# Kernel tuning notes

Hardware: AMD Instinct MI355X
Metric: run time of the kernel (lower is better)

Reference implementation:

```python
import jax, jax.numpy as jnp
import numpy as np

B, L, D, H = 2, 2048, 1024, 16
HD = D // H  # head_dim = 64


def setup_inputs() -> dict:
    key = jax.random.key(0)
    k1, k2, k3 = jax.random.split(key, 3)
    x = jax.random.normal(k1, (B, L, D), dtype=jnp.float32)
    # nn.Linear(d_model, 3*d_model): weight [3D, D], bias [3D]
    lim = 1.0 / np.sqrt(D)
    W_qkv = jax.random.uniform(k2, (3 * D, D), dtype=jnp.float32, minval=-lim, maxval=lim)
    b_qkv = jax.random.uniform(k3, (3 * D,), dtype=jnp.float32, minval=-lim, maxval=lim)
    return {"x": x, "W_qkv": W_qkv, "b_qkv": b_qkv}


def reference(x, W_qkv, b_qkv):
    b, l, d = x.shape
    qkv = x @ W_qkv.T + b_qkv                      # [b, l, 3d]
    q, k, v = jnp.split(qkv, 3, axis=-1)           # each [b, l, d]
    # split heads: [b, l, h, hd]
    q = q.reshape(b, l, H, HD)
    k = k.reshape(b, l, H, HD)
    v = v.reshape(b, l, H, HD)
    scale = 1.0 / np.sqrt(HD).astype(np.float32)
    # scores [b, h, l, l]
    scores = jnp.einsum('bqhd,bkhd->bhqk', q, k) * scale
    attn = jax.nn.softmax(scores, axis=-1)
    out = jnp.einsum('bhqk,bkhd->bqhd', attn, v)   # [b, l, h, hd]
    return out.reshape(b, l, d)
```

## Files before the change

kernel.cpp:

```cpp
#include <hip/hip_runtime.h>

#define BATCH 2
#define SEQ 2048
#define DMODEL 1024
#define NH 16
#define HD 64
#define M_TOT (BATCH*SEQ)
#define N_TOT (3*DMODEL)
#define K_TOT (DMODEL)
#define NQK   (2*DMODEL)
#define QSCALE 0.18033688011112042f

typedef __attribute__((ext_vector_type(8)))  _Float16 f16x8;
typedef __attribute__((ext_vector_type(4)))  float    f32x4;
typedef __attribute__((ext_vector_type(16))) float    f32x16;

static __device__ __forceinline__ unsigned short f2h(float f) {
  _Float16 h = (_Float16)f;
  return __builtin_bit_cast(unsigned short, h);
}

static __device__ __forceinline__ f32x16 zero16() {
  f32x16 z;
  #pragma unroll
  for (int i = 0; i < 16; ++i) z[i] = 0.f;
  return z;
}

static __device__ __forceinline__ void async16(const unsigned short* g, unsigned short* l) {
  __builtin_amdgcn_global_load_lds(
      (const __attribute__((address_space(1))) unsigned*)g,
      (__attribute__((address_space(3))) unsigned*)l, 16, 0, 0);
}

__global__ __launch_bounds__(256) void cast_f16(
    const float* __restrict__ src, unsigned short* __restrict__ dst, int n8)
{
  int i = blockIdx.x * 256 + threadIdx.x;
  if (i >= n8) return;
  float4 v0 = ((const float4*)src)[2*i];
  float4 v1 = ((const float4*)src)[2*i + 1];
  uint4 pk;
  pk.x = (unsigned)f2h(v0.x) | ((unsigned)f2h(v0.y) << 16);
  pk.y = (unsigned)f2h(v0.z) | ((unsigned)f2h(v0.w) << 16);
  pk.z = (unsigned)f2h(v1.x) | ((unsigned)f2h(v1.y) << 16);
  pk.w = (unsigned)f2h(v1.z) | ((unsigned)f2h(v1.w) << 16);
  ((uint4*)dst)[i] = pk;
}

__global__ __launch_bounds__(256) void qkv_gemm_mfma(
    const unsigned short* __restrict__ Xh,
    const unsigned short* __restrict__ Wh,
    const float* __restrict__ bias,
    unsigned short* __restrict__ QK,
    unsigned short* __restrict__ VT)
{
  __shared__ unsigned short As[128][64];
  __shared__ unsigned short Bs[128][64];

  const int tid  = threadIdx.x;
  const int wave = tid >> 6;
  const int lane = tid & 63;
  const int l15  = lane & 15;
  const int quad = lane >> 4;

  const bool isV = (blockIdx.x >= (NQK/128));
  const int n0 = (isV ? (blockIdx.x - NQK/128) : blockIdx.x) * 128;
  const int m0 = blockIdx.y * 128;

  const unsigned short* Arows = isV ? (Wh + (size_t)(NQK + n0) * K_TOT)
                                    : (Xh + (size_t)m0 * K_TOT);
  const unsigned short* Brows = isV ? (Xh + (size_t)m0 * K_TOT)
                                    : (Wh + (size_t)n0 * K_TOT);

  const int sr = tid >> 3;
  const int sp = tid & 7;
  const int sg = ((sp - sr) & 7) * 8;

  const int wm = (wave & 1) * 64;
  const int wn = (wave >> 1) * 64;

  f32x4 acc[4][4];
  #pragma unroll
  for (int i = 0; i < 4; ++i)
    #pragma unroll
    for (int j = 0; j < 4; ++j) acc[i][j] = (f32x4){0.f,0.f,0.f,0.f};

  for (int k0 = 0; k0 < K_TOT; k0 += 64) {
    __syncthreads();
    #pragma unroll
    for (int s = 0; s < 4; ++s) {
      async16(Arows + (size_t)(s*32 + sr) * K_TOT + k0 + sg, &As[0][0] + s*2048 + tid*8);
      async16(Brows + (size_t)(s*32 + sr) * K_TOT + k0 + sg, &Bs[0][0] + s*2048 + tid*8);
    }
    __syncthreads();

    #pragma unroll
    for (int h = 0; h < 2; ++h) {
      f16x8 af[4], bf[4];
      #pragma unroll
      for (int i = 0; i < 4; ++i) {
        const int r = wm + i*16 + l15;
        af[i] = *(const f16x8*)&As[r][((h*4 + quad + r) & 7) * 8];
      }
      #pragma unroll
      for (int j = 0; j < 4; ++j) {
        const int r = wn + j*16 + l15;
        bf[j] = *(const f16x8*)&Bs[r][((h*4 + quad + r) & 7) * 8];
      }
      #pragma unroll
      for (int i = 0; i < 4; ++i)
        #pragma unroll
        for (int j = 0; j < 4; ++j)
          acc[i][j] = __builtin_amdgcn_mfma_f32_16x16x32_f16(af[i], bf[j], acc[i][j], 0, 0, 0);
    }
  }

  if (!isV) {
    const float sc = (n0 < DMODEL) ? QSCALE : 1.0f;
    float bv[4];
    #pragma unroll
    for (int j = 0; j < 4; ++j) bv[j] = bias[n0 + wn + j*16 + l15];
    #pragma unroll
    for (int i = 0; i < 4; ++i)
      #pragma unroll
      for (int j = 0; j < 4; ++j)
        #pragma unroll
        for (int r = 0; r < 4; ++r) {
          const size_t row = (size_t)(m0 + wm + i*16 + quad*4 + r);
          QK[row * NQK + n0 + wn + j*16 + l15] = f2h((acc[i][j][r] + bv[j]) * sc);
        }
  } else {
    const int bidx  = m0 >> 11;
    const int sbase = (m0 & 2047) + wn;
    #pragma unroll
    for (int i = 0; i < 4; ++i)
      #pragma unroll
      for (int r = 0; r < 4; ++r) {
        const int nn = n0 + wm + i*16 + quad*4 + r;
        const float bb = bias[NQK + nn];
        unsigned short* drow =
            VT + ((size_t)(bidx*NH + (nn >> 6)) * HD + (nn & 63)) * SEQ + sbase;
        #pragma unroll
        for (int j = 0; j < 4; ++j)
          drow[j*16 + l15] = f2h(acc[i][j][r] + bb);
      }
  }
}

__global__ __launch_bounds__(256) void attn_mfma3(
    const unsigned short* __restrict__ QK,
    const unsigned short* __restrict__ VT,
    float* __restrict__ out)
{
  __shared__ unsigned short Ks[2][64][64];
  __shared__ unsigned short Vs[2][64][64];
  __shared__ unsigned short Ps[4][32][72];
  __shared__ float Dn[4][32];

  const int tid  = threadIdx.x;
  const int wv   = tid >> 6;
  const int lane = tid & 63;
  const int l31  = lane & 31;
  const int h32  = lane >> 5;
  const int qsw  = l31 >> 3;

  const int qt = blockIdx.x;
  const int hh = blockIdx.y;
  const int b  = blockIdx.z;
  const int q0 = qt*128 + wv*32;

  f16x8 qf[4];
  {
    const unsigned short* qrow = QK + (size_t)(b*SEQ + q0 + l31) * NQK + hh*HD;
    #pragma unroll
    for (int f = 0; f < 4; ++f)
      qf[f] = *(const f16x8*)(qrow + f*16 + h32*8);
  }

  const unsigned short* Kg = QK + (size_t)b*SEQ*NQK + DMODEL + hh*HD;
  const unsigned short* Vg = VT + (size_t)(b*NH + hh) * HD * SEQ;

  const int sr = tid >> 3;
  const int sp = tid & 7;
  const int sg = ((sp - sr) & 7) * 8;

  const unsigned short* kg0 = Kg + (size_t)sr      * NQK + sg;
  const unsigned short* kg1 = Kg + (size_t)(sr+32) * NQK + sg;
  const unsigned short* vg0 = Vg + (size_t)sr      * SEQ + sg;
  const unsigned short* vg1 = Vg + (size_t)(sr+32) * SEQ + sg;
  unsigned short* kl = &Ks[0][0][0] + tid*8;
  unsigned short* vl = &Vs[0][0][0] + tid*8;

  f32x16 oacc[2];
  oacc[0] = zero16();
  oacc[1] = zero16();
  float dsum = 0.f;

  auto STAGE = [&](int kt, int bb) {
    const size_t krow = (size_t)kt * 64 * NQK;
    const int    kcol = kt * 64;
    async16(kg0 + krow, kl + bb*4096);
    async16(kg1 + krow, kl + bb*4096 + 2048);
    async16(vg0 + kcol, vl + bb*4096);
    async16(vg1 + kcol, vl + bb*4096 + 2048);
  };

  auto COMPUTE = [&](int bb) {
    const unsigned short* ks = &Ks[bb][0][0];
    const unsigned short* vs = &Vs[bb][0][0];

    f32x16 sa[2];
    sa[0] = zero16();
    sa[1] = zero16();
    __builtin_amdgcn_s_setprio(1);
    #pragma unroll
    for (int f = 0; f < 4; ++f) {
      const int g = f*2 + h32;
      #pragma unroll
      for (int kb = 0; kb < 2; ++kb) {
        const int row = kb*32 + l31;
        f16x8 kf = *(const f16x8*)(ks + row*64 + ((g + row) & 7) * 8);
        sa[kb] = __builtin_amdgcn_mfma_f32_32x32x16_f16(kf, qf[f], sa[kb], 0, 0, 0);
      }
    }
    __builtin_amdgcn_s_setprio(0);

    #pragma unroll
    for (int kb = 0; kb < 2; ++kb) {
      #pragma unroll
      for (int g4 = 0; g4 < 4; ++g4) {
        unsigned short hsv[4];
        #pragma unroll
        for (int r = 0; r < 4; ++r) {
          float p = exp2f(sa[kb][g4*4 + r]);
          dsum += p;
          hsv[r] = f2h(p);
        }
        unsigned short* dst =
            &Ps[wv][l31][(((kb*4 + g4) ^ qsw) & 7) * 8 + h32*4];
        uint2 pk;
        pk.x = (unsigned)hsv[0] | ((unsigned)hsv[1] << 16);
        pk.y = (unsigned)hsv[2] | ((unsigned)hsv[3] << 16);
        *(uint2*)dst = pk;
      }
    }

    __builtin_amdgcn_s_setprio(1);
    #pragma unroll
    for (int f = 0; f < 4; ++f) {
      const int g = f*2 + h32;
      f16x8 pf = *(const f16x8*)&Ps[wv][l31][((g ^ qsw) & 7) * 8];
      #pragma unroll
      for (int jd = 0; jd < 2; ++jd) {
        const int row = jd*32 + l31;
        f16x8 vf = *(const f16x8*)(vs + row*64 + ((g + row) & 7) * 8);
        oacc[jd] = __builtin_amdgcn_mfma_f32_32x32x16_f16(pf, vf, oacc[jd], 0, 0, 0);
      }
    }
    __builtin_amdgcn_s_setprio(0);
  };

  STAGE(0, 0);
  for (int kt = 0; kt < SEQ/64 - 1; ++kt) {
    STAGE(kt + 1, (kt + 1) & 1);
    asm volatile("s_waitcnt vmcnt(4)" ::: "memory");
    __builtin_amdgcn_s_barrier();
    COMPUTE(kt & 1);
    asm volatile("" ::: "memory");
    __builtin_amdgcn_s_barrier();
  }
  asm volatile("s_waitcnt vmcnt(0)" ::: "memory");
  __builtin_amdgcn_s_barrier();
  COMPUTE((SEQ/64 - 1) & 1);

  dsum += __shfl_xor(dsum, 32, 64);
  Dn[wv][l31] = 1.f / dsum;

  #pragma unroll
  for (int jd = 0; jd < 2; ++jd) {
    #pragma unroll
    for (int g4 = 0; g4 < 4; ++g4) {
      #pragma unroll
      for (int r = 0; r < 4; ++r) {
        const int qrow = g4*8 + h32*4 + r;
        const float oval = oacc[jd][g4*4 + r] * Dn[wv][qrow];
        out[(size_t)(b*SEQ + q0 + qrow) * DMODEL + hh*HD + jd*32 + l31] = oval;
      }
    }
  }
}

extern "C" void kernel_launch(void* const* d_in, const int* in_sizes, int n_in,
                              void* d_out, int out_size, void* d_ws, size_t ws_size,
                              hipStream_t stream) {
  const float* x    = (const float*)d_in[0];
  const float* W    = (const float*)d_in[1];
  const float* bias = (const float*)d_in[2];
  float* out = (float*)d_out;

  unsigned short* qk = (unsigned short*)d_ws;
  unsigned short* vt = qk + (size_t)M_TOT * NQK;
  unsigned short* xh = vt + (size_t)BATCH * NH * HD * SEQ;
  unsigned short* wh = xh + (size_t)M_TOT * K_TOT;

  cast_f16<<<(M_TOT*K_TOT/8 + 255)/256, 256, 0, stream>>>(x, xh, M_TOT*K_TOT/8);
  cast_f16<<<(N_TOT*K_TOT/8 + 255)/256, 256, 0, stream>>>(W, wh, N_TOT*K_TOT/8);

  dim3 g1(N_TOT/128, M_TOT/128);
  qkv_gemm_mfma<<<g1, 256, 0, stream>>>(xh, wh, bias, qk, vt);

  dim3 g2(SEQ/128, NH, BATCH);
  attn_mfma3<<<g2, 256, 0, stream>>>(qk, vt, out);
}
```

Measured before the change: 186.3 us.

## Double-buffer QKV GEMM K-loop and pass P via lane shuffles instead of LDS

```diff
diff --git a/kernel.cpp b/kernel.cpp
--- a/kernel.cpp
+++ b/kernel.cpp
@@ -18,6 +18,10 @@
 static __device__ __forceinline__ unsigned short f2h(float f) {
   _Float16 h = (_Float16)f;
   return __builtin_bit_cast(unsigned short, h);
+}
+
+static __device__ __forceinline__ unsigned pk2h(float a, float b) {
+  return (unsigned)f2h(a) | ((unsigned)f2h(b) << 16);
 }
 
 static __device__ __forceinline__ f32x16 zero16() {
@@ -55,8 +59,8 @@
     unsigned short* __restrict__ QK,
     unsigned short* __restrict__ VT)
 {
-  __shared__ unsigned short As[128][64];
-  __shared__ unsigned short Bs[128][64];
+  __shared__ unsigned short As[2][128][32];
+  __shared__ unsigned short Bs[2][128][32];
 
   const int tid  = threadIdx.x;
   const int wave = tid >> 6;
@@ -73,9 +77,14 @@
   const unsigned short* Brows = isV ? (Xh + (size_t)m0 * K_TOT)
                                     : (Wh + (size_t)n0 * K_TOT);
 
-  const int sr = tid >> 3;
-  const int sp = tid & 7;
-  const int sg = ((sp - sr) & 7) * 8;
+  const int srow = tid >> 2;
+  const int skc  = (tid & 3) * 8;
+  const unsigned short* Ag0 = Arows + (size_t)srow * K_TOT + skc;
+  const unsigned short* Ag1 = Arows + (size_t)(64 + srow) * K_TOT + skc;
+  const unsigned short* Bg0 = Brows + (size_t)srow * K_TOT + skc;
+  const unsigned short* Bg1 = Brows + (size_t)(64 + srow) * K_TOT + skc;
+  unsigned short* Al = &As[0][0][0] + tid * 8;
+  unsigned short* Bl = &Bs[0][0][0] + tid * 8;
 
   const int wm = (wave & 1) * 64;
   const int wn = (wave >> 1) * 64;
@@ -86,35 +95,41 @@
     #pragma unroll
     for (int j = 0; j < 4; ++j) acc[i][j] = (f32x4){0.f,0.f,0.f,0.f};
 
-  for (int k0 = 0; k0 < K_TOT; k0 += 64) {
-    __syncthreads();
-    #pragma unroll
-    for (int s = 0; s < 4; ++s) {
-      async16(Arows + (size_t)(s*32 + sr) * K_TOT + k0 + sg, &As[0][0] + s*2048 + tid*8);
-      async16(Brows + (size_t)(s*32 + sr) * K_TOT + k0 + sg, &Bs[0][0] + s*2048 + tid*8);
-    }
-    __syncthreads();
-
-    #pragma unroll
-    for (int h = 0; h < 2; ++h) {
-      f16x8 af[4], bf[4];
-      #pragma unroll
-      for (int i = 0; i < 4; ++i) {
-        const int r = wm + i*16 + l15;
-        af[i] = *(const f16x8*)&As[r][((h*4 + quad + r) & 7) * 8];
-      }
-      #pragma unroll
-      for (int j = 0; j < 4; ++j) {
-        const int r = wn + j*16 + l15;
-        bf[j] = *(const f16x8*)&Bs[r][((h*4 + quad + r) & 7) * 8];
-      }
-      #pragma unroll
-      for (int i = 0; i < 4; ++i)
-        #pragma unroll
-        for (int j = 0; j < 4; ++j)
-          acc[i][j] = __builtin_amdgcn_mfma_f32_16x16x32_f16(af[i], bf[j], acc[i][j], 0, 0, 0);
-    }
-  }
+  auto STAGE = [&](int k0, int bb) {
+    async16(Ag0 + k0, Al + bb*4096);
+    async16(Ag1 + k0, Al + bb*4096 + 2048);
+    async16(Bg0 + k0, Bl + bb*4096);
+    async16(Bg1 + k0, Bl + bb*4096 + 2048);
+  };
+
+  auto COMPUTE = [&](int bb) {
+    f16x8 af[4], bf[4];
+    #pragma unroll
+    for (int i = 0; i < 4; ++i)
+      af[i] = *(const f16x8*)&As[bb][wm + i*16 + l15][quad*8];
+    #pragma unroll
+    for (int j = 0; j < 4; ++j)
+      bf[j] = *(const f16x8*)&Bs[bb][wn + j*16 + l15][quad*8];
+    __builtin_amdgcn_s_setprio(1);
+    #pragma unroll
+    for (int i = 0; i < 4; ++i)
+      #pragma unroll
+      for (int j = 0; j < 4; ++j)
+        acc[i][j] = __builtin_amdgcn_mfma_f32_16x16x32_f16(af[i], bf[j], acc[i][j], 0, 0, 0);
+    __builtin_amdgcn_s_setprio(0);
+  };
+
+  STAGE(0, 0);
+  for (int t = 0; t < K_TOT/32 - 1; ++t) {
+    STAGE((t+1)*32, (t+1) & 1);
+    asm volatile("s_waitcnt vmcnt(4)" ::: "memory");
+    __builtin_amdgcn_s_barrier();
+    COMPUTE(t & 1);
+    __builtin_amdgcn_s_barrier();
+  }
+  asm volatile("s_waitcnt vmcnt(0)" ::: "memory");
+  __builtin_amdgcn_s_barrier();
+  COMPUTE((K_TOT/32 - 1) & 1);
 
   if (!isV) {
     const float sc = (n0 < DMODEL) ? QSCALE : 1.0f;
@@ -155,7 +170,6 @@
 {
   __shared__ unsigned short Ks[2][64][64];
   __shared__ unsigned short Vs[2][64][64];
-  __shared__ unsigned short Ps[4][32][72];
   __shared__ float Dn[4][32];
 
   const int tid  = threadIdx.x;
@@ -163,7 +177,6 @@
   const int lane = tid & 63;
   const int l31  = lane & 31;
   const int h32  = lane >> 5;
-  const int qsw  = l31 >> 3;
 
   const int qt = blockIdx.x;
   const int hh = blockIdx.y;
@@ -227,30 +240,32 @@
     __builtin_amdgcn_s_setprio(0);
 
     #pragma unroll
-    for (int kb = 0; kb < 2; ++kb) {
-      #pragma unroll
-      for (int g4 = 0; g4 < 4; ++g4) {
-        unsigned short hsv[4];
-        #pragma unroll
-        for (int r = 0; r < 4; ++r) {
-          float p = exp2f(sa[kb][g4*4 + r]);
-          dsum += p;
-          hsv[r] = f2h(p);
-        }
-        unsigned short* dst =
-            &Ps[wv][l31][(((kb*4 + g4) ^ qsw) & 7) * 8 + h32*4];
-        uint2 pk;
-        pk.x = (unsigned)hsv[0] | ((unsigned)hsv[1] << 16);
-        pk.y = (unsigned)hsv[2] | ((unsigned)hsv[3] << 16);
-        *(uint2*)dst = pk;
-      }
-    }
+    for (int kb = 0; kb < 2; ++kb)
+      #pragma unroll
+      for (int i = 0; i < 16; ++i) {
+        float p = exp2f(sa[kb][i]);
+        dsum += p;
+        sa[kb][i] = p;
+      }
 
     __builtin_amdgcn_s_setprio(1);
     #pragma unroll
     for (int f = 0; f < 4; ++f) {
+      const int kb = f >> 1;
+      const int ge = (f & 1) * 2;
+      unsigned A = pk2h(sa[kb][ge*4+0], sa[kb][ge*4+1]);
+      unsigned B = pk2h(sa[kb][ge*4+2], sa[kb][ge*4+3]);
+      unsigned C = pk2h(sa[kb][ge*4+4], sa[kb][ge*4+5]);
+      unsigned D = pk2h(sa[kb][ge*4+6], sa[kb][ge*4+7]);
+      unsigned t0 = (unsigned)__shfl_xor((int)(h32 ? A : C), 32, 64);
+      unsigned t1 = (unsigned)__shfl_xor((int)(h32 ? B : D), 32, 64);
+      uint4 pw;
+      pw.x = h32 ? t0 : A;
+      pw.y = h32 ? t1 : B;
+      pw.z = h32 ? C : t0;
+      pw.w = h32 ? D : t1;
+      f16x8 pf = __builtin_bit_cast(f16x8, pw);
       const int g = f*2 + h32;
-      f16x8 pf = *(const f16x8*)&Ps[wv][l31][((g ^ qsw) & 7) * 8];
       #pragma unroll
       for (int jd = 0; jd < 2; ++jd) {
         const int row = jd*32 + l31;
@@ -267,7 +282,6 @@
     asm volatile("s_waitcnt vmcnt(4)" ::: "memory");
     __builtin_amdgcn_s_barrier();
     COMPUTE(kt & 1);
-    asm volatile("" ::: "memory");
     __builtin_amdgcn_s_barrier();
   }
   asm volatile("s_waitcnt vmcnt(0)" ::: "memory");
```

Result: slower. 192.6 us (+3.4%).

## Triple-buffer GEMM and attention K/V loads, merge the two cast kernels

Applied to the files above, without the earlier changes.

```diff
diff --git a/kernel.cpp b/kernel.cpp
--- a/kernel.cpp
+++ b/kernel.cpp
@@ -33,19 +33,34 @@
       (__attribute__((address_space(3))) unsigned*)l, 16, 0, 0);
 }
 
-__global__ __launch_bounds__(256) void cast_f16(
-    const float* __restrict__ src, unsigned short* __restrict__ dst, int n8)
+static __device__ __forceinline__ void barrier_fenced() {
+  asm volatile("" ::: "memory");
+  __builtin_amdgcn_sched_barrier(0);
+  __builtin_amdgcn_s_barrier();
+  __builtin_amdgcn_sched_barrier(0);
+  asm volatile("" ::: "memory");
+}
+
+__global__ __launch_bounds__(256) void cast_f16_2(
+    const float* __restrict__ xsrc, const float* __restrict__ wsrc,
+    unsigned short* __restrict__ xdst, unsigned short* __restrict__ wdst,
+    int n8x, int n8tot)
 {
   int i = blockIdx.x * 256 + threadIdx.x;
-  if (i >= n8) return;
-  float4 v0 = ((const float4*)src)[2*i];
-  float4 v1 = ((const float4*)src)[2*i + 1];
+  if (i >= n8tot) return;
+  const float* src;
+  unsigned short* dst;
+  int idx;
+  if (i < n8x) { src = xsrc; dst = xdst; idx = i; }
+  else         { src = wsrc; dst = wdst; idx = i - n8x; }
+  float4 v0 = ((const float4*)src)[2*idx];
+  float4 v1 = ((const float4*)src)[2*idx + 1];
   uint4 pk;
   pk.x = (unsigned)f2h(v0.x) | ((unsigned)f2h(v0.y) << 16);
   pk.y = (unsigned)f2h(v0.z) | ((unsigned)f2h(v0.w) << 16);
   pk.z = (unsigned)f2h(v1.x) | ((unsigned)f2h(v1.y) << 16);
   pk.w = (unsigned)f2h(v1.z) | ((unsigned)f2h(v1.w) << 16);
-  ((uint4*)dst)[i] = pk;
+  ((uint4*)dst)[idx] = pk;
 }
 
 __global__ __launch_bounds__(256) void qkv_gemm_mfma(
@@ -55,8 +70,8 @@
     unsigned short* __restrict__ QK,
     unsigned short* __restrict__ VT)
 {
-  __shared__ unsigned short As[128][64];
-  __shared__ unsigned short Bs[128][64];
+  __shared__ unsigned short As[3][128][32];
+  __shared__ unsigned short Bs[3][128][32];
 
   const int tid  = threadIdx.x;
   const int wave = tid >> 6;
@@ -73,9 +88,14 @@
   const unsigned short* Brows = isV ? (Xh + (size_t)m0 * K_TOT)
                                     : (Wh + (size_t)n0 * K_TOT);
 
-  const int sr = tid >> 3;
-  const int sp = tid & 7;
-  const int sg = ((sp - sr) & 7) * 8;
+  const int srow = tid >> 2;
+  const int skc  = (tid & 3) * 8;
+  const unsigned short* Ag0 = Arows + (size_t)srow * K_TOT + skc;
+  const unsigned short* Ag1 = Arows + (size_t)(64 + srow) * K_TOT + skc;
+  const unsigned short* Bg0 = Brows + (size_t)srow * K_TOT + skc;
+  const unsigned short* Bg1 = Brows + (size_t)(64 + srow) * K_TOT + skc;
+  unsigned short* Al = &As[0][0][0] + tid * 8;
+  unsigned short* Bl = &Bs[0][0][0] + tid * 8;
 
   const int wm = (wave & 1) * 64;
   const int wn = (wave >> 1) * 64;
@@ -86,35 +106,46 @@
     #pragma unroll
     for (int j = 0; j < 4; ++j) acc[i][j] = (f32x4){0.f,0.f,0.f,0.f};
 
-  for (int k0 = 0; k0 < K_TOT; k0 += 64) {
-    __syncthreads();
-    #pragma unroll
-    for (int s = 0; s < 4; ++s) {
-      async16(Arows + (size_t)(s*32 + sr) * K_TOT + k0 + sg, &As[0][0] + s*2048 + tid*8);
-      async16(Brows + (size_t)(s*32 + sr) * K_TOT + k0 + sg, &Bs[0][0] + s*2048 + tid*8);
-    }
-    __syncthreads();
-
-    #pragma unroll
-    for (int h = 0; h < 2; ++h) {
-      f16x8 af[4], bf[4];
-      #pragma unroll
-      for (int i = 0; i < 4; ++i) {
-        const int r = wm + i*16 + l15;
-        af[i] = *(const f16x8*)&As[r][((h*4 + quad + r) & 7) * 8];
-      }
-      #pragma unroll
-      for (int j = 0; j < 4; ++j) {
-        const int r = wn + j*16 + l15;
-        bf[j] = *(const f16x8*)&Bs[r][((h*4 + quad + r) & 7) * 8];
-      }
-      #pragma unroll
-      for (int i = 0; i < 4; ++i)
-        #pragma unroll
-        for (int j = 0; j < 4; ++j)
-          acc[i][j] = __builtin_amdgcn_mfma_f32_16x16x32_f16(af[i], bf[j], acc[i][j], 0, 0, 0);
-    }
-  }
+  auto STAGE = [&](int k0, int bb) {
+    async16(Ag0 + k0, Al + bb*4096);
+    async16(Ag1 + k0, Al + bb*4096 + 2048);
+    async16(Bg0 + k0, Bl + bb*4096);
+    async16(Bg1 + k0, Bl + bb*4096 + 2048);
+  };
+
+  auto COMPUTE = [&](int bb) {
+    f16x8 af[4], bf[4];
+    #pragma unroll
+    for (int i = 0; i < 4; ++i)
+      af[i] = *(const f16x8*)&As[bb][wm + i*16 + l15][quad*8];
+    #pragma unroll
+    for (int j = 0; j < 4; ++j)
+      bf[j] = *(const f16x8*)&Bs[bb][wn + j*16 + l15][quad*8];
+    #pragma unroll
+    for (int i = 0; i < 4; ++i)
+      #pragma unroll
+      for (int j = 0; j < 4; ++j)
+        acc[i][j] = __builtin_amdgcn_mfma_f32_16x16x32_f16(af[i], bf[j], acc[i][j], 0, 0, 0);
+  };
+
+  STAGE(0, 0);
+  STAGE(32, 1);
+  int bs = 2, bc = 0;
+  for (int t = 0; t < K_TOT/32 - 2; ++t) {
+    asm volatile("s_waitcnt vmcnt(4)" ::: "memory");
+    barrier_fenced();
+    STAGE((t+2)*32, bs);
+    COMPUTE(bc);
+    bs = (bs == 2) ? 0 : bs + 1;
+    bc = (bc == 2) ? 0 : bc + 1;
+  }
+  asm volatile("s_waitcnt vmcnt(4)" ::: "memory");
+  barrier_fenced();
+  COMPUTE(bc);
+  bc = (bc == 2) ? 0 : bc + 1;
+  asm volatile("s_waitcnt vmcnt(0)" ::: "memory");
+  barrier_fenced();
+  COMPUTE(bc);
 
   if (!isV) {
     const float sc = (n0 < DMODEL) ? QSCALE : 1.0f;
@@ -153,8 +184,8 @@
     const unsigned short* __restrict__ VT,
     float* __restrict__ out)
 {
-  __shared__ unsigned short Ks[2][64][64];
-  __shared__ unsigned short Vs[2][64][64];
+  __shared__ unsigned short Ks[3][64][64];
+  __shared__ unsigned short Vs[3][64][64];
   __shared__ unsigned short Ps[4][32][72];
   __shared__ float Dn[4][32];
 
@@ -262,17 +293,23 @@
   };
 
   STAGE(0, 0);
-  for (int kt = 0; kt < SEQ/64 - 1; ++kt) {
-    STAGE(kt + 1, (kt + 1) & 1);
+  STAGE(1, 1);
+  int bs = 2, bc = 0;
+  for (int kt = 0; kt < SEQ/64 - 2; ++kt) {
     asm volatile("s_waitcnt vmcnt(4)" ::: "memory");
-    __builtin_amdgcn_s_barrier();
-    COMPUTE(kt & 1);
-    asm volatile("" ::: "memory");
-    __builtin_amdgcn_s_barrier();
-  }
+    barrier_fenced();
+    STAGE(kt + 2, bs);
+    COMPUTE(bc);
+    bs = (bs == 2) ? 0 : bs + 1;
+    bc = (bc == 2) ? 0 : bc + 1;
+  }
+  asm volatile("s_waitcnt vmcnt(4)" ::: "memory");
+  barrier_fenced();
+  COMPUTE(bc);
+  bc = (bc == 2) ? 0 : bc + 1;
   asm volatile("s_waitcnt vmcnt(0)" ::: "memory");
-  __builtin_amdgcn_s_barrier();
-  COMPUTE((SEQ/64 - 1) & 1);
+  barrier_fenced();
+  COMPUTE(bc);
 
   dsum += __shfl_xor(dsum, 32, 64);
   Dn[wv][l31] = 1.f / dsum;
@@ -304,8 +341,9 @@
   unsigned short* xh = vt + (size_t)BATCH * NH * HD * SEQ;
   unsigned short* wh = xh + (size_t)M_TOT * K_TOT;
 
-  cast_f16<<<(M_TOT*K_TOT/8 + 255)/256, 256, 0, stream>>>(x, xh, M_TOT*K_TOT/8);
-  cast_f16<<<(N_TOT*K_TOT/8 + 255)/256, 256, 0, stream>>>(W, wh, N_TOT*K_TOT/8);
+  const int n8x = M_TOT*K_TOT/8;
+  const int n8w = N_TOT*K_TOT/8;
+  cast_f16_2<<<(n8x + n8w + 255)/256, 256, 0, stream>>>(x, W, xh, wh, n8x, n8x + n8w);
 
   dim3 g1(N_TOT/128, M_TOT/128);
   qkv_gemm_mfma<<<g1, 256, 0, stream>>>(xh, wh, bias, qk, vt);
```

Measured after the change: 187.6 us. Within noise of the previous version (+0.7%).
